# Optimization experiments

Hardware: AMD Instinct MI355X
Metric: run time of the kernel (lower is better)

Reference implementation:

```python
import jax, jax.numpy as jnp
import numpy as np

B, C, H, W = 4, 64, 192, 192
G = 8           # offset groups per input stream
OFF_CH = 27 * G # 216 channels in each offset input
MAG = 10.0
KH = KW = 3
PAD = 1


def setup_inputs() -> dict:
    key = jax.random.key(0)
    ks = jax.random.split(key, 7)
    rn = lambda k, s, sc=1.0: jax.random.normal(k, s, dtype=jnp.float32) * sc
    return {
        "x1": rn(ks[0], (B, C, H, W)),
        "offset1": rn(ks[1], (B, OFF_CH, H, W)),
        "flow1": rn(ks[2], (B, 2, H, W), 2.0),
        "x2": rn(ks[3], (B, C, H, W)),
        "offset2": rn(ks[4], (B, OFF_CH, H, W)),
        "flow2": rn(ks[5], (B, 2, H, W), 2.0),
        "weight": rn(ks[6], (C, (2 * C) // (2 * G), KH, KW), 0.05),  # groups = 16
        "bias": jnp.zeros((C,), jnp.float32),
    }


def _prep(out, flow, magnitude):
    # chunk into (o1, o2, mask) along channels
    o1, o2, m = jnp.split(out, 3, axis=1)
    mask = jax.nn.sigmoid(m)
    off = jnp.tanh(jnp.concatenate([o1, o2], axis=1)) * magnitude
    rep = off.shape[1] // 2
    # flow.flip(1).repeat(1, rep, 1, 1) -> tile the 2-channel (fy, fx) pattern
    off = off + jnp.tile(flow[:, ::-1], (1, rep, 1, 1))
    return off, mask


def _deform_conv(x, offset, mask, weight, bias):
    # x: [B, Cin, H, W]; offset: [B, 2*n_off*9, H, W]; mask: [B, n_off*9, H, W]
    b, cin, h, w = x.shape
    n_off = 2 * G                      # 16 offset groups == 16 weight groups
    cg = cin // n_off                  # channels per group (8)
    K = KH * KW
    off = offset.reshape(b, n_off, K, 2, h, w)
    m = mask.reshape(b, n_off, K, h, w)
    k = jnp.arange(K)
    ki = (k // KW).astype(x.dtype)
    kj = (k % KW).astype(x.dtype)
    ys = jnp.arange(h, dtype=x.dtype)
    xs = jnp.arange(w, dtype=x.dtype)
    # sampling positions [B, n_off, K, H, W]; (dy, dx) channel order as torchvision
    py = off[:, :, :, 0] + ki[None, None, :, None, None] + (ys - PAD)[None, None, None, :, None]
    px = off[:, :, :, 1] + kj[None, None, :, None, None] + (xs - PAD)[None, None, None, None, :]
    y0 = jnp.floor(py)
    x0 = jnp.floor(px)
    wy = py - y0
    wx = px - x0
    x_r = x.reshape(b, n_off, cg, h * w)
    val = jnp.zeros((b, n_off, cg, K, h, w), x.dtype)
    # bilinear gather, zero outside image (4 fixed corners)
    corners = [(y0, x0, (1 - wy) * (1 - wx)), (y0, x0 + 1, (1 - wy) * wx),
               (y0 + 1, x0, wy * (1 - wx)), (y0 + 1, x0 + 1, wy * wx)]
    for yc, xc, wgt in corners:
        valid = ((yc >= 0) & (yc <= h - 1) & (xc >= 0) & (xc <= w - 1)).astype(x.dtype)
        yi = jnp.clip(yc, 0, h - 1).astype(jnp.int32)
        xi = jnp.clip(xc, 0, w - 1).astype(jnp.int32)
        idx = (yi * w + xi).reshape(b, n_off, 1, K * h * w)
        gat = jnp.take_along_axis(x_r, idx, axis=3).reshape(b, n_off, cg, K, h, w)
        val = val + gat * (wgt * valid)[:, :, None]
    val = val * m[:, :, None]          # modulation
    cout = weight.shape[0]
    og = cout // n_off                 # out channels per group (4)
    w_r = weight.reshape(n_off, og, cg, K)
    out = jnp.einsum('bgckhw,gock->bgohw', val, w_r).reshape(b, cout, h, w)
    return out + bias[None, :, None, None]


def reference(x1, offset1, flow1, x2, offset2, flow2, weight, bias):
    o1, m1 = _prep(offset1, flow1, MAG)
    o2, m2 = _prep(offset2, flow2, MAG)
    x = jnp.concatenate([x1, x2], axis=1)
    off = jnp.concatenate([o1, o2], axis=1)
    msk = jnp.concatenate([m1, m2], axis=1)
    return _deform_conv(x, off, msk, weight, bias)
```

## Files before the change

kernel.cpp:

```cpp
#include <hip/hip_runtime.h>

#define H 192
#define W 192
#define HW (192 * 192)

typedef _Float16 half2_t __attribute__((ext_vector_type(2)));

__device__ __forceinline__ float frcp(float x) { return __builtin_amdgcn_rcpf(x); }
__device__ __forceinline__ float ftanh(float x) {
    float t = __expf(x * 2.0f);
    return 1.0f - 2.0f * frcp(t + 1.0f);
}
__device__ __forceinline__ float fsigmoid(float x) {
    return frcp(1.0f + __expf(-x));
}
__device__ __forceinline__ half2_t splat(float v) {
    _Float16 h = (_Float16)v;
    half2_t r = {h, h};
    return r;
}

__global__ __launch_bounds__(256)
void transpose_x(const float* __restrict__ x1, const float* __restrict__ x2,
                 uint4* __restrict__ xt)
{
    const int pix = blockIdx.x * 256 + threadIdx.x;
    const int bg  = blockIdx.y;
    const int b = bg >> 4, gg = bg & 15;
    const int s = gg >> 3, g = gg & 7;
    const float* xb = (s ? x2 : x1) + (size_t)(b * 64 + g * 8) * HW + pix;
    unsigned w0[4];
#pragma unroll
    for (int j = 0; j < 4; ++j) {
        half2_t h = {(_Float16)xb[(size_t)(2 * j) * HW],
                     (_Float16)xb[(size_t)(2 * j + 1) * HW]};
        w0[j] = __builtin_bit_cast(unsigned, h);
    }
    xt[(size_t)bg * HW + pix] = make_uint4(w0[0], w0[1], w0[2], w0[3]);
}

__global__ __launch_bounds__(256, 4)
void dcn_gather(const float* __restrict__ off1, const float* __restrict__ flow1,
                const float* __restrict__ off2, const float* __restrict__ flow2,
                const float* __restrict__ wgt, const float* __restrict__ bias,
                const uint4* __restrict__ xt, float* __restrict__ out)
{
    const int t_raw = blockIdx.x;
    const int tile  = (t_raw & 7) * 18 + (t_raw >> 3);
    const int gg   = blockIdx.y;
    const int b    = blockIdx.z;
    const int tilex = tile % 6, tiley = tile / 6;
    const int lx = threadIdx.x & 31, ly = threadIdx.x >> 5;
    const int x = tilex * 32 + lx;
    const int y = tiley * 8 + ly;
    const int pix = y * W + x;

    __shared__ half2_t wsh2[9][4][4];
    for (int i = threadIdx.x; i < 144; i += 256) {
        const int k = i >> 4, r = i & 15, j = r >> 2, o = r & 3;
        const float lo = wgt[gg * 288 + o * 72 + (2 * j) * 9 + k];
        const float hi = wgt[gg * 288 + o * 72 + (2 * j + 1) * 9 + k];
        wsh2[k][j][o] = half2_t{(_Float16)lo, (_Float16)hi};
    }
    __syncthreads();

    const int s = gg >> 3;
    const int g = gg & 7;
    const float* ob = (s ? off2 : off1) + (size_t)b * 216 * HW + pix;
    const float* fb = (s ? flow2 : flow1) + (size_t)b * 2 * HW + pix;
    const uint4* tb = xt + (size_t)(b * 16 + gg) * HW;

    float rdy[9], rdx[9], rm[9];
#pragma unroll
    for (int k = 0; k < 9; ++k) {
        const int t = g * 9 + k;
        rdy[k] = ob[(size_t)(2 * t) * HW];
        rdx[k] = ob[(size_t)(2 * t + 1) * HW];
        rm[k]  = ob[(size_t)(144 + t) * HW];
    }
    const float f0 = fb[0];
    const float f1 = fb[HW];

    int     idc[9][4];
    half2_t hw00[9], hw01[9], hw10[9], hw11[9];
#pragma unroll
    for (int k = 0; k < 9; ++k) {
        const float mk = fsigmoid(rm[k]);
        const float py = ftanh(rdy[k]) * 10.0f + f1 + (float)(k / 3 + y - 1);
        const float px = ftanh(rdx[k]) * 10.0f + f0 + (float)(k % 3 + x - 1);
        const float fy0 = floorf(py);
        const float fx0 = floorf(px);
        const float wy = py - fy0;
        const float wx = px - fx0;
        const int y0 = (int)fy0, x0 = (int)fx0;
        const int y1 = y0 + 1, x1i = x0 + 1;
        const bool vy0 = (unsigned)y0  < (unsigned)H;
        const bool vy1 = (unsigned)y1  < (unsigned)H;
        const bool vx0 = (unsigned)x0  < (unsigned)W;
        const bool vx1 = (unsigned)x1i < (unsigned)W;
        float w00 = (1.0f - wy) * (1.0f - wx) * mk;
        float w01 = (1.0f - wy) * wx * mk;
        float w10 = wy * (1.0f - wx) * mk;
        float w11 = wy * wx * mk;
        hw00[k] = splat((vy0 && vx0) ? w00 : 0.0f);
        hw01[k] = splat((vy0 && vx1) ? w01 : 0.0f);
        hw10[k] = splat((vy1 && vx0) ? w10 : 0.0f);
        hw11[k] = splat((vy1 && vx1) ? w11 : 0.0f);
        const int iy0 = min(max(y0, 0), H - 1);
        const int iy1 = min(max(y1, 0), H - 1);
        const int ix0 = min(max(x0, 0), W - 1);
        const int ix1 = min(max(x1i, 0), W - 1);
        idc[k][0] = iy0 * W + ix0;
        idc[k][1] = iy0 * W + ix1;
        idc[k][2] = iy1 * W + ix0;
        idc[k][3] = iy1 * W + ix1;
    }

    float acc0 = bias[gg * 4 + 0];
    float acc1 = bias[gg * 4 + 1];
    float acc2 = bias[gg * 4 + 2];
    float acc3 = bias[gg * 4 + 3];

#pragma unroll
    for (int k = 0; k < 9; ++k) {
        const uint4 q00 = tb[idc[k][0]];
        const uint4 q01 = tb[idc[k][1]];
        const uint4 q10 = tb[idc[k][2]];
        const uint4 q11 = tb[idc[k][3]];
        const half2_t* A = (const half2_t*)&q00;
        const half2_t* Bq = (const half2_t*)&q01;
        const half2_t* Cq = (const half2_t*)&q10;
        const half2_t* Dq = (const half2_t*)&q11;
#pragma unroll
        for (int j = 0; j < 4; ++j) {
            half2_t vb = hw00[k] * A[j];
            vb = hw01[k] * Bq[j] + vb;
            vb = hw10[k] * Cq[j] + vb;
            vb = hw11[k] * Dq[j] + vb;
            half2_t w0 = wsh2[k][j][0];
            half2_t w1 = wsh2[k][j][1];
            half2_t w2 = wsh2[k][j][2];
            half2_t w3 = wsh2[k][j][3];
            acc0 = __builtin_amdgcn_fdot2(vb, w0, acc0, false);
            acc1 = __builtin_amdgcn_fdot2(vb, w1, acc1, false);
            acc2 = __builtin_amdgcn_fdot2(vb, w2, acc2, false);
            acc3 = __builtin_amdgcn_fdot2(vb, w3, acc3, false);
        }
    }

    float* op = out + ((size_t)(b * 64 + gg * 4)) * HW + pix;
    op[0 * HW] = acc0;
    op[1 * HW] = acc1;
    op[2 * HW] = acc2;
    op[3 * HW] = acc3;
}

__global__ __launch_bounds__(256)
void dcn_fused(const float* __restrict__ x1, const float* __restrict__ off1,
               const float* __restrict__ flow1, const float* __restrict__ x2,
               const float* __restrict__ off2, const float* __restrict__ flow2,
               const float* __restrict__ wgt, const float* __restrict__ bias,
               float* __restrict__ out)
{
    const int tile = blockIdx.x;
    const int gg   = blockIdx.y;
    const int b    = blockIdx.z;
    const int tilex = tile % 6, tiley = tile / 6;
    const int lx = threadIdx.x & 31, ly = threadIdx.x >> 5;
    const int x = tilex * 32 + lx;
    const int y = tiley * 8 + ly;
    const int pix = y * W + x;

    __shared__ float wsh[9][8][4];
    for (int i = threadIdx.x; i < 288; i += 256) {
        int o = i / 72;
        int r = i - o * 72;
        int c = r / 9;
        int k = r - c * 9;
        wsh[k][c][o] = wgt[gg * 288 + i];
    }
    __syncthreads();

    const int s = gg >> 3;
    const int g = gg & 7;
    const float* xb = (s ? x2 : x1) + (size_t)(b * 64 + g * 8) * HW;
    const float* ob = (s ? off2 : off1) + (size_t)b * 216 * HW;
    const float* fb = (s ? flow2 : flow1) + (size_t)b * 2 * HW;

    const float f0 = fb[pix];
    const float f1 = fb[HW + pix];

    float acc0 = bias[gg * 4 + 0];
    float acc1 = bias[gg * 4 + 1];
    float acc2 = bias[gg * 4 + 2];
    float acc3 = bias[gg * 4 + 3];

    for (int k = 0; k < 9; ++k) {
        const int t = g * 9 + k;
        const float rdy = ob[(size_t)(2 * t) * HW + pix];
        const float rdx = ob[(size_t)(2 * t + 1) * HW + pix];
        const float rm  = ob[(size_t)(144 + t) * HW + pix];
        const float mk = fsigmoid(rm);
        const float py = ftanh(rdy) * 10.0f + f1 + (float)(k / 3 + y - 1);
        const float px = ftanh(rdx) * 10.0f + f0 + (float)(k % 3 + x - 1);
        const float fy0 = floorf(py);
        const float fx0 = floorf(px);
        const float wy = py - fy0;
        const float wx = px - fx0;
        const int y0 = (int)fy0, x0 = (int)fx0;
        const int y1 = y0 + 1, x1i = x0 + 1;
        const bool vy0 = (unsigned)y0  < (unsigned)H;
        const bool vy1 = (unsigned)y1  < (unsigned)H;
        const bool vx0 = (unsigned)x0  < (unsigned)W;
        const bool vx1 = (unsigned)x1i < (unsigned)W;
        float w00 = (1.0f - wy) * (1.0f - wx) * mk;
        float w01 = (1.0f - wy) * wx * mk;
        float w10 = wy * (1.0f - wx) * mk;
        float w11 = wy * wx * mk;
        w00 = (vy0 && vx0) ? w00 : 0.0f;
        w01 = (vy0 && vx1) ? w01 : 0.0f;
        w10 = (vy1 && vx0) ? w10 : 0.0f;
        w11 = (vy1 && vx1) ? w11 : 0.0f;
        const int iy0 = min(max(y0, 0), H - 1);
        const int iy1 = min(max(y1, 0), H - 1);
        const int ix0 = min(max(x0, 0), W - 1);
        const int ix1 = min(max(x1i, 0), W - 1);
        const int o00 = iy0 * W + ix0;
        const int o01 = iy0 * W + ix1;
        const int o10 = iy1 * W + ix0;
        const int o11 = iy1 * W + ix1;
#pragma unroll
        for (int c = 0; c < 8; ++c) {
            const float* p = xb + (size_t)c * HW;
            const float v = p[o00] * w00 + p[o01] * w01 + p[o10] * w10 + p[o11] * w11;
            acc0 = fmaf(wsh[k][c][0], v, acc0);
            acc1 = fmaf(wsh[k][c][1], v, acc1);
            acc2 = fmaf(wsh[k][c][2], v, acc2);
            acc3 = fmaf(wsh[k][c][3], v, acc3);
        }
    }

    float* op = out + ((size_t)(b * 64 + gg * 4)) * HW + pix;
    op[0 * HW] = acc0;
    op[1 * HW] = acc1;
    op[2 * HW] = acc2;
    op[3 * HW] = acc3;
}

extern "C" void kernel_launch(void* const* d_in, const int* in_sizes, int n_in,
                              void* d_out, int out_size, void* d_ws, size_t ws_size,
                              hipStream_t stream) {
    const float* x1    = (const float*)d_in[0];
    const float* off1  = (const float*)d_in[1];
    const float* flow1 = (const float*)d_in[2];
    const float* x2    = (const float*)d_in[3];
    const float* off2  = (const float*)d_in[4];
    const float* flow2 = (const float*)d_in[5];
    const float* wgt   = (const float*)d_in[6];
    const float* bias  = (const float*)d_in[7];
    float* out = (float*)d_out;

    const size_t need = (size_t)4 * 16 * HW * 8 * 2;
    if (ws_size >= need) {
        uint4* xt = (uint4*)d_ws;
        transpose_x<<<dim3(HW / 256, 64, 1), 256, 0, stream>>>(x1, x2, xt);
        dcn_gather<<<dim3(144, 16, 4), 256, 0, stream>>>(off1, flow1, off2, flow2,
                                                         wgt, bias, xt, out);
    } else {
        dcn_fused<<<dim3(144, 16, 4), 256, 0, stream>>>(x1, off1, flow1, x2, off2,
                                                        flow2, wgt, bias, out);
    }
}
```

Measured before the change: 199.1 us.

## Software-pipeline bilinear gathers with sched barriers in dcn_gather

```diff
diff --git a/kernel.cpp b/kernel.cpp
--- a/kernel.cpp
+++ b/kernel.cpp
@@ -39,7 +39,7 @@
     xt[(size_t)bg * HW + pix] = make_uint4(w0[0], w0[1], w0[2], w0[3]);
 }
 
-__global__ __launch_bounds__(256, 4)
+__global__ __launch_bounds__(256, 3)
 void dcn_gather(const float* __restrict__ off1, const float* __restrict__ flow1,
                 const float* __restrict__ off2, const float* __restrict__ flow2,
                 const float* __restrict__ wgt, const float* __restrict__ bias,
@@ -81,72 +81,83 @@
     const float f0 = fb[0];
     const float f1 = fb[HW];
 
-    int     idc[9][4];
-    half2_t hw00[9], hw01[9], hw10[9], hw11[9];
-#pragma unroll
-    for (int k = 0; k < 9; ++k) {
-        const float mk = fsigmoid(rm[k]);
-        const float py = ftanh(rdy[k]) * 10.0f + f1 + (float)(k / 3 + y - 1);
-        const float px = ftanh(rdx[k]) * 10.0f + f0 + (float)(k % 3 + x - 1);
-        const float fy0 = floorf(py);
-        const float fx0 = floorf(px);
-        const float wy = py - fy0;
-        const float wx = px - fx0;
-        const int y0 = (int)fy0, x0 = (int)fx0;
-        const int y1 = y0 + 1, x1i = x0 + 1;
-        const bool vy0 = (unsigned)y0  < (unsigned)H;
-        const bool vy1 = (unsigned)y1  < (unsigned)H;
-        const bool vx0 = (unsigned)x0  < (unsigned)W;
-        const bool vx1 = (unsigned)x1i < (unsigned)W;
-        float w00 = (1.0f - wy) * (1.0f - wx) * mk;
-        float w01 = (1.0f - wy) * wx * mk;
-        float w10 = wy * (1.0f - wx) * mk;
-        float w11 = wy * wx * mk;
-        hw00[k] = splat((vy0 && vx0) ? w00 : 0.0f);
-        hw01[k] = splat((vy0 && vx1) ? w01 : 0.0f);
-        hw10[k] = splat((vy1 && vx0) ? w10 : 0.0f);
-        hw11[k] = splat((vy1 && vx1) ? w11 : 0.0f);
-        const int iy0 = min(max(y0, 0), H - 1);
-        const int iy1 = min(max(y1, 0), H - 1);
-        const int ix0 = min(max(x0, 0), W - 1);
-        const int ix1 = min(max(x1i, 0), W - 1);
-        idc[k][0] = iy0 * W + ix0;
-        idc[k][1] = iy0 * W + ix1;
-        idc[k][2] = iy1 * W + ix0;
-        idc[k][3] = iy1 * W + ix1;
-    }
-
     float acc0 = bias[gg * 4 + 0];
     float acc1 = bias[gg * 4 + 1];
     float acc2 = bias[gg * 4 + 2];
     float acc3 = bias[gg * 4 + 3];
 
-#pragma unroll
-    for (int k = 0; k < 9; ++k) {
-        const uint4 q00 = tb[idc[k][0]];
-        const uint4 q01 = tb[idc[k][1]];
-        const uint4 q10 = tb[idc[k][2]];
-        const uint4 q11 = tb[idc[k][3]];
-        const half2_t* A = (const half2_t*)&q00;
-        const half2_t* Bq = (const half2_t*)&q01;
-        const half2_t* Cq = (const half2_t*)&q10;
-        const half2_t* Dq = (const half2_t*)&q11;
-#pragma unroll
-        for (int j = 0; j < 4; ++j) {
-            half2_t vb = hw00[k] * A[j];
-            vb = hw01[k] * Bq[j] + vb;
-            vb = hw10[k] * Cq[j] + vb;
-            vb = hw11[k] * Dq[j] + vb;
-            half2_t w0 = wsh2[k][j][0];
-            half2_t w1 = wsh2[k][j][1];
-            half2_t w2 = wsh2[k][j][2];
-            half2_t w3 = wsh2[k][j][3];
-            acc0 = __builtin_amdgcn_fdot2(vb, w0, acc0, false);
-            acc1 = __builtin_amdgcn_fdot2(vb, w1, acc1, false);
-            acc2 = __builtin_amdgcn_fdot2(vb, w2, acc2, false);
-            acc3 = __builtin_amdgcn_fdot2(vb, w3, acc3, false);
-        }
-    }
+    half2_t hA[2][4], hB[2][4], hC[2][4], hD[2][4], hE[1][4];
+    uint4   qA[2][4], qB[2][4], qC[2][4], qD[2][4], qE[1][4];
+
+#define PREP(K0, NT, HX, QX)                                                   \
+    _Pragma("unroll")                                                          \
+    for (int u = 0; u < (NT); ++u) {                                           \
+        const int k = (K0) + u;                                                \
+        const float mk = fsigmoid(rm[k]);                                      \
+        const float py = ftanh(rdy[k]) * 10.0f + f1 + (float)(k / 3 + y - 1);  \
+        const float px = ftanh(rdx[k]) * 10.0f + f0 + (float)(k % 3 + x - 1);  \
+        const float fy0 = floorf(py);                                          \
+        const float fx0 = floorf(px);                                          \
+        const float wy = py - fy0;                                             \
+        const float wx = px - fx0;                                             \
+        const int y0 = (int)fy0, x0 = (int)fx0;                                \
+        const bool vy0 = (unsigned)y0       < (unsigned)H;                     \
+        const bool vy1 = (unsigned)(y0 + 1) < (unsigned)H;                     \
+        const bool vx0 = (unsigned)x0       < (unsigned)W;                     \
+        const bool vx1 = (unsigned)(x0 + 1) < (unsigned)W;                     \
+        HX[u][0] = splat((vy0 && vx0) ? (1.0f - wy) * (1.0f - wx) * mk : 0.0f);\
+        HX[u][1] = splat((vy0 && vx1) ? (1.0f - wy) * wx * mk : 0.0f);         \
+        HX[u][2] = splat((vy1 && vx0) ? wy * (1.0f - wx) * mk : 0.0f);         \
+        HX[u][3] = splat((vy1 && vx1) ? wy * wx * mk : 0.0f);                  \
+        const int iy0 = min(max(y0, 0), H - 1);                                \
+        const int iy1 = min(max(y0 + 1, 0), H - 1);                            \
+        const int ix0 = min(max(x0, 0), W - 1);                                \
+        const int ix1 = min(max(x0 + 1, 0), W - 1);                            \
+        QX[u][0] = tb[iy0 * W + ix0];                                          \
+        QX[u][1] = tb[iy0 * W + ix1];                                          \
+        QX[u][2] = tb[iy1 * W + ix0];                                          \
+        QX[u][3] = tb[iy1 * W + ix1];                                          \
+    }
+
+#define PROC(K0, NT, HX, QX)                                                   \
+    _Pragma("unroll")                                                          \
+    for (int u = 0; u < (NT); ++u) {                                           \
+        const int k = (K0) + u;                                                \
+        const half2_t* A  = (const half2_t*)&QX[u][0];                         \
+        const half2_t* Bq = (const half2_t*)&QX[u][1];                         \
+        const half2_t* Cq = (const half2_t*)&QX[u][2];                         \
+        const half2_t* Dq = (const half2_t*)&QX[u][3];                         \
+        _Pragma("unroll")                                                      \
+        for (int j = 0; j < 4; ++j) {                                          \
+            half2_t vb = HX[u][0] * A[j];                                      \
+            vb = HX[u][1] * Bq[j] + vb;                                        \
+            vb = HX[u][2] * Cq[j] + vb;                                        \
+            vb = HX[u][3] * Dq[j] + vb;                                        \
+            acc0 = __builtin_amdgcn_fdot2(vb, wsh2[k][j][0], acc0, false);     \
+            acc1 = __builtin_amdgcn_fdot2(vb, wsh2[k][j][1], acc1, false);     \
+            acc2 = __builtin_amdgcn_fdot2(vb, wsh2[k][j][2], acc2, false);     \
+            acc3 = __builtin_amdgcn_fdot2(vb, wsh2[k][j][3], acc3, false);     \
+        }                                                                      \
+    }
+
+    PREP(0, 2, hA, qA)
+    PREP(2, 2, hB, qB)
+    __builtin_amdgcn_sched_barrier(0);
+    PROC(0, 2, hA, qA)
+    PREP(4, 2, hC, qC)
+    __builtin_amdgcn_sched_barrier(0);
+    PROC(2, 2, hB, qB)
+    PREP(6, 2, hD, qD)
+    __builtin_amdgcn_sched_barrier(0);
+    PROC(4, 2, hC, qC)
+    PREP(8, 1, hE, qE)
+    __builtin_amdgcn_sched_barrier(0);
+    PROC(6, 2, hD, qD)
+    __builtin_amdgcn_sched_barrier(0);
+    PROC(8, 1, hE, qE)
+
+#undef PREP
+#undef PROC
 
     float* op = out + ((size_t)(b * 64 + gg * 4)) * HW + pix;
     op[0 * HW] = acc0;
```

Result: no change. 199.4 us (+0.2%).
